# Performance work log

Measured on AMD Instinct MI355X. Metric: run time of the kernel, lower is better.

## Reference

```python
import math
import jax, jax.numpy as jnp
import numpy as np

CAPACITY = 2097152  # 2**21, power of two -> complete sum tree
SIZE = 1048576


def _build_tree(probs):
    # Tree layout: node i has children 2i+1, 2i+2; leaves are tree[-capacity:].
    # For power-of-two capacity this is levels concatenated root-first.
    levels = [probs]
    x = probs
    while x.shape[0] > 1:
        x = x.reshape(-1, 2).sum(axis=1)
        levels.append(x)
    return jnp.concatenate(levels[::-1])


def setup_inputs() -> dict:
    key = jax.random.key(0)
    k1, k2 = jax.random.split(key)
    priorities = jax.random.uniform(k1, (CAPACITY,), dtype=jnp.float32)
    uniform = jax.random.uniform(k2, (SIZE,), dtype=jnp.float32)
    return {"priorities": priorities, "uniform": uniform, "size": SIZE}


def reference(priorities, uniform, size):
    cap = priorities.shape[0]
    depth = int(math.log2(cap))  # number of traversal steps (complete tree)
    tree = _build_tree(priorities)  # [2*cap - 1]
    total = tree[0]

    # sample() with equal_mode=True: stratified samples in [0, total)
    offsets = jnp.linspace(0.0, total, size + 1, dtype=jnp.float32)[:-1]
    sums = uniform * total / size + offsets  # [size]
    idx0 = jnp.zeros((size,), dtype=jnp.int32)

    def body(_, carry):
        idx, s = carry
        left = 2 * idx + 1
        left_val = tree[left]            # gather [size]
        go_left = s <= left_val
        idx = jnp.where(go_left, left, left + 1)
        s = jnp.where(go_left, s, s - left_val)
        return idx, s

    idx, _ = jax.lax.fori_loop(0, depth, body, (idx0, sums))
    return idx - cap + 1  # leaf index in [0, cap)
```

## Files before the change

kernel.cpp:

```cpp
#include <hip/hip_runtime.h>


#define CAP   2097152
#define NSAMP 1048576

__global__ __launch_bounds__(256) void build_lower(const float* __restrict__ prio,
                                                   float* __restrict__ tree) {
    __shared__ float bufA[2048];
    __shared__ float bufB[1024];
    const int b = blockIdx.x;
    const int t = threadIdx.x;

    const float4* p4 = (const float4*)(prio + (size_t)b * 4096);
    #pragma unroll
    for (int q = 0; q < 4; ++q) {
        float4 a = p4[t * 4 + q];
        bufA[t * 8 + q * 2 + 0] = a.x + a.y;
        bufA[t * 8 + q * 2 + 1] = a.z + a.w;
    }
    __syncthreads();
    {
        float* g = tree + ((1 << 20) - 1) + b * 2048;
        #pragma unroll
        for (int i = t; i < 2048; i += 256) g[i] = bufA[i];
    }

    float* src = bufA;
    float* dst = bufB;
    int cnt = 1024;
    int off = (1 << 19) - 1;
    for (int lvl = 19; lvl >= 9; --lvl) {
        for (int i = t; i < cnt; i += 256) {
            float2 v = ((const float2*)src)[i];
            float r = v.x + v.y;
            dst[i] = r;
            tree[off + b * cnt + i] = r;
        }
        __syncthreads();
        float* tmp = src; src = dst; dst = tmp;
        off = (off - 1) >> 1;
        cnt >>= 1;
    }
}

__global__ __launch_bounds__(256) void build_upper(float* __restrict__ tree) {
    __shared__ float bufA[512];
    __shared__ float bufB[256];
    const int t = threadIdx.x;
    bufA[t]       = tree[511 + t];
    bufA[t + 256] = tree[511 + t + 256];
    __syncthreads();
    float* src = bufA;
    float* dst = bufB;
    int cnt = 256;
    int off = 255;
    for (int lvl = 8; lvl >= 0; --lvl) {
        for (int i = t; i < cnt; i += 256) {
            float2 v = ((const float2*)src)[i];
            float r = v.x + v.y;
            dst[i] = r;
            tree[off + i] = r;
        }
        __syncthreads();
        float* tmp = src; src = dst; dst = tmp;
        off = (off - 1) >> 1;
        cnt >>= 1;
    }
}

__global__ __launch_bounds__(256) void sample_kernel(const float* __restrict__ tree,
                                                     const float* __restrict__ prio,
                                                     const float* __restrict__ uniform,
                                                     int* __restrict__ out) {
    const int j = blockIdx.x * 256 + threadIdx.x;
    const float total = tree[0];
    const float scale = total / (float)NSAMP;
    float s = uniform[j] * total / (float)NSAMP + scale * (float)j;

    int idx = 0;
    #pragma unroll
    for (int d = 0; d < 20; ++d) {
        int left = 2 * idx + 1;
        float lv = tree[left];
        bool right = (s > lv);
        s = right ? (s - lv) : s;
        idx = right ? (left + 1) : left;
    }
    int left = 2 * idx + 1;
    float lv = prio[left - (CAP - 1)];
    idx = (s > lv) ? (left + 1) : left;
    out[j] = idx - (CAP - 1);
}

extern "C" void kernel_launch(void* const* d_in, const int* in_sizes, int n_in,
                              void* d_out, int out_size, void* d_ws, size_t ws_size,
                              hipStream_t stream) {
    const float* prio    = (const float*)d_in[0];
    const float* uniform = (const float*)d_in[1];
    (void)in_sizes; (void)n_in; (void)out_size; (void)ws_size;

    float* tree = (float*)d_ws;

    build_lower<<<512, 256, 0, stream>>>(prio, tree);
    build_upper<<<1, 256, 0, stream>>>(tree);
    sample_kernel<<<NSAMP / 256, 256, 0, stream>>>(tree, prio, uniform, (int*)d_out);
}
```

Measured before the change: 86.24 us.

## Truncate stored tree, cache top levels in LDS, recompute bottom levels from priorities

The build kernel now stores only levels 0-18 (minus the top, which each sample block recomputes), cutting global writes by about fourfold. The single-block upper-build kernel is removed: each sampling block loads levels 9-12 into shared memory and reduces the top 9 levels itself, then runs the first 12 traversal steps from LDS. The last three levels are recomputed from two float4 loads of the priorities, and each thread handles four samples to add memory-level parallelism. The cost is redundant top-of-tree work in every block, about 32KB of LDS per block, and float summation order that may differ slightly from the reference.

```diff
diff --git a/kernel.cpp b/kernel.cpp
--- a/kernel.cpp
+++ b/kernel.cpp
@@ -1,35 +1,33 @@
 #include <hip/hip_runtime.h>
 
 
-#define CAP   2097152
-#define NSAMP 1048576
+#define CAP    (1 << 21)
+#define NSAMP  (1 << 20)
+#define L18OFF ((1 << 18) - 1)
 
-__global__ __launch_bounds__(256) void build_lower(const float* __restrict__ prio,
-                                                   float* __restrict__ tree) {
-    __shared__ float bufA[2048];
-    __shared__ float bufB[1024];
-    const int b = blockIdx.x;
-    const int t = threadIdx.x;
+__global__ __launch_bounds__(256) void build_tree(const float* __restrict__ prio,
+                                                  float* __restrict__ tree) {
+    __shared__ __align__(16) float A[512];
+    __shared__ __align__(16) float B[256];
+    const int b = blockIdx.x, t = threadIdx.x;
+    const float4* p4 = (const float4*)(prio + (size_t)b * 4096);
 
-    const float4* p4 = (const float4*)(prio + (size_t)b * 4096);
     #pragma unroll
-    for (int q = 0; q < 4; ++q) {
-        float4 a = p4[t * 4 + q];
-        bufA[t * 8 + q * 2 + 0] = a.x + a.y;
-        bufA[t * 8 + q * 2 + 1] = a.z + a.w;
+    for (int i = t; i < 512; i += 256) {
+        float4 x = p4[2 * i], y = p4[2 * i + 1];
+        A[i] = ((x.x + x.y) + (x.z + x.w)) + ((y.x + y.y) + (y.z + y.w));
     }
     __syncthreads();
     {
-        float* g = tree + ((1 << 20) - 1) + b * 2048;
+        float* g = tree + L18OFF + b * 512;
         #pragma unroll
-        for (int i = t; i < 2048; i += 256) g[i] = bufA[i];
+        for (int i = t; i < 512; i += 256) g[i] = A[i];
     }
-
-    float* src = bufA;
-    float* dst = bufB;
-    int cnt = 1024;
-    int off = (1 << 19) - 1;
-    for (int lvl = 19; lvl >= 9; --lvl) {
+    float* src = A;
+    float* dst = B;
+    int cnt = 256;
+    int off = (1 << 17) - 1;
+    for (int lvl = 17; lvl >= 9; --lvl) {
         for (int i = t; i < cnt; i += 256) {
             float2 v = ((const float2*)src)[i];
             float r = v.x + v.y;
@@ -43,53 +41,78 @@
     }
 }
 
-__global__ __launch_bounds__(256) void build_upper(float* __restrict__ tree) {
-    __shared__ float bufA[512];
-    __shared__ float bufB[256];
-    const int t = threadIdx.x;
-    bufA[t]       = tree[511 + t];
-    bufA[t + 256] = tree[511 + t + 256];
-    __syncthreads();
-    float* src = bufA;
-    float* dst = bufB;
-    int cnt = 256;
-    int off = 255;
-    for (int lvl = 8; lvl >= 0; --lvl) {
-        for (int i = t; i < cnt; i += 256) {
-            float2 v = ((const float2*)src)[i];
-            float r = v.x + v.y;
-            dst[i] = r;
-            tree[off + i] = r;
-        }
-        __syncthreads();
-        float* tmp = src; src = dst; dst = tmp;
-        off = (off - 1) >> 1;
-        cnt >>= 1;
-    }
-}
-
 __global__ __launch_bounds__(256) void sample_kernel(const float* __restrict__ tree,
                                                      const float* __restrict__ prio,
                                                      const float* __restrict__ uniform,
                                                      int* __restrict__ out) {
-    const int j = blockIdx.x * 256 + threadIdx.x;
-    const float total = tree[0];
+    __shared__ float nds[8191];
+    const int t = threadIdx.x;
+
+    for (int i = 511 + t; i < 8191; i += 256) nds[i] = tree[i];
+    __syncthreads();
+    {
+        int cnt = 256, off = 255;
+        for (int lvl = 8; lvl >= 0; --lvl) {
+            for (int i = t; i < cnt; i += 256) {
+                int n = off + i;
+                nds[n] = nds[2 * n + 1] + nds[2 * n + 2];
+            }
+            __syncthreads();
+            off = (off - 1) >> 1;
+            cnt >>= 1;
+        }
+    }
+
+    const float total = nds[0];
     const float scale = total / (float)NSAMP;
-    float s = uniform[j] * total / (float)NSAMP + scale * (float)j;
+    const int base = blockIdx.x * 1024 + t;
 
-    int idx = 0;
+    float s[4];
+    int   id[4];
     #pragma unroll
-    for (int d = 0; d < 20; ++d) {
-        int left = 2 * idx + 1;
-        float lv = tree[left];
-        bool right = (s > lv);
-        s = right ? (s - lv) : s;
-        idx = right ? (left + 1) : left;
+    for (int q = 0; q < 4; ++q) {
+        int j = base + 256 * q;
+        s[q]  = uniform[j] * total / (float)NSAMP + scale * (float)j;
+        id[q] = 0;
     }
-    int left = 2 * idx + 1;
-    float lv = prio[left - (CAP - 1)];
-    idx = (s > lv) ? (left + 1) : left;
-    out[j] = idx - (CAP - 1);
+
+    #pragma unroll
+    for (int d = 0; d < 12; ++d) {
+        #pragma unroll
+        for (int q = 0; q < 4; ++q) {
+            int left = 2 * id[q] + 1;
+            float lv = nds[left];
+            bool r = s[q] > lv;
+            s[q]  = r ? s[q] - lv : s[q];
+            id[q] = r ? left + 1 : left;
+        }
+    }
+    #pragma unroll
+    for (int d = 0; d < 6; ++d) {
+        #pragma unroll
+        for (int q = 0; q < 4; ++q) {
+            int left = 2 * id[q] + 1;
+            float lv = tree[left];
+            bool r = s[q] > lv;
+            s[q]  = r ? s[q] - lv : s[q];
+            id[q] = r ? left + 1 : left;
+        }
+    }
+    #pragma unroll
+    for (int q = 0; q < 4; ++q) {
+        int p = id[q] - L18OFF;
+        const float4* pp = (const float4*)prio + 2 * (size_t)p;
+        float4 x = pp[0], y = pp[1];
+        float l19 = (x.x + x.y) + (x.z + x.w);
+        bool r1 = s[q] > l19;
+        float ss = r1 ? s[q] - l19 : s[q];
+        float l20 = r1 ? (y.x + y.y) : (x.x + x.y);
+        bool r2 = ss > l20;
+        ss = r2 ? ss - l20 : ss;
+        float leaf = r1 ? (r2 ? y.z : y.x) : (r2 ? x.z : x.x);
+        bool r3 = ss > leaf;
+        out[base + 256 * q] = 8 * p + (r1 ? 4 : 0) + (r2 ? 2 : 0) + (r3 ? 1 : 0);
+    }
 }
 
 extern "C" void kernel_launch(void* const* d_in, const int* in_sizes, int n_in,
@@ -101,7 +124,6 @@
 
     float* tree = (float*)d_ws;
 
-    build_lower<<<512, 256, 0, stream>>>(prio, tree);
-    build_upper<<<1, 256, 0, stream>>>(tree);
-    sample_kernel<<<NSAMP / 256, 256, 0, stream>>>(tree, prio, uniform, (int*)d_out);
+    build_tree<<<512, 256, 0, stream>>>(prio, tree);
+    sample_kernel<<<NSAMP / 1024, 256, 0, stream>>>(tree, prio, uniform, (int*)d_out);
 }
```

Result: faster. 76.26 us, median of 2 (-11.6%).
